# Kernel tuning notes

Hardware: AMD Instinct MI355X
Metric: run time of the kernel (lower is better)

The kernel has to match this reference:

```python
import jax, jax.numpy as jnp
import numpy as np

S, B, D, H = 2048, 2, 1024, 16
DK = D // H
SCALE = 1.0 / np.sqrt(DK)


def setup_inputs() -> dict:
    key = jax.random.key(0)
    ks = jax.random.split(key, 12)
    std = 1.0 / np.sqrt(D)
    inp = {
        "query": jax.random.normal(ks[0], (S, B, D), jnp.float32),
        "key": jax.random.normal(ks[1], (S, B, D), jnp.float32),
        "value": jax.random.normal(ks[2], (S, B, D), jnp.float32),
        # causal mask [S, S, 1]; mask[i, j] = 1 iff query i may attend key j
        "mask": jnp.tril(jnp.ones((S, S), jnp.bool_))[:, :, None],
        "Wq": jax.random.normal(ks[3], (D, D), jnp.float32) * std,
        "bq": jax.random.normal(ks[4], (D,), jnp.float32) * std,
        "Wk": jax.random.normal(ks[5], (D, D), jnp.float32) * std,
        "bk": jax.random.normal(ks[6], (D,), jnp.float32) * std,
        "Wv": jax.random.normal(ks[7], (D, D), jnp.float32) * std,
        "bv": jax.random.normal(ks[8], (D,), jnp.float32) * std,
        "Wo": jax.random.normal(ks[9], (D, D), jnp.float32) * std,
        "bo": jax.random.normal(ks[10], (D,), jnp.float32) * std,
    }
    return inp


def _proj(x, W, b):
    # nn.Linear: x @ W.T + b, then split into heads -> [S, B, H, DK]
    s, bsz, _ = x.shape
    y = jnp.einsum('sbd,ed->sbe', x, W) + b
    return y.reshape(s, bsz, H, DK)


def reference(query, key, value, mask, Wq, bq, Wk, bk, Wv, bv, Wo, bo):
    q = _proj(query, Wq, bq)   # [S,B,H,DK]
    k = _proj(key, Wk, bk)
    v = _proj(value, Wv, bv)
    scores = jnp.einsum('ibhd,jbhd->ijbh', q, k) * SCALE  # [S,S,B,H]
    m = mask[:, :, :, None]  # [S,S,1,1] or [S,S,B,1]
    scores = jnp.where(m, scores, jnp.float32(-1e9))
    attn = jax.nn.softmax(scores, axis=1)
    x = jnp.einsum('ijbh,jbhd->ibhd', attn, v)  # [S,B,H,DK]
    x = x.reshape(S, B, D)
    return jnp.einsum('sbd,ed->sbe', x, Wo) + bo
```

## Files before the change

### kernel.cpp

```cpp
#include <hip/hip_runtime.h>
#include <stdint.h>

#define S_LEN 2048
#define BATCH 2
#define DMODEL 1024
#define NHEAD 16
#define DHEAD 64
#define SCALE 0.125f

typedef float f32x4 __attribute__((ext_vector_type(4)));
typedef float f32x16 __attribute__((ext_vector_type(16)));
typedef __bf16 bf16x8 __attribute__((ext_vector_type(8)));

__device__ __forceinline__ unsigned short f2bf(float f) {
  union { float f; unsigned int u; } v;
  v.f = f;
  unsigned int u = v.u;
  return (unsigned short)((u + 0x7fffu + ((u >> 16) & 1u)) >> 16);
}

__device__ __forceinline__ void gld16(const void* g, void* l) {
  __builtin_amdgcn_global_load_lds((__attribute__((address_space(1))) void*)(g),
                                   (__attribute__((address_space(3))) void*)(l),
                                   16, 0, 0);
}

__global__ void cvt_all_kernel(const float* __restrict__ q, const float* __restrict__ k,
                               const float* __restrict__ v, const float* __restrict__ wq,
                               const float* __restrict__ wk, const float* __restrict__ wv,
                               const float* __restrict__ wosrc, unsigned short* __restrict__ xp,
                               unsigned short* __restrict__ wp, unsigned short* __restrict__ wo) {
  const int b = blockIdx.x;
  const float* src;
  unsigned short* dst;
  if (b < 12288) {
    const int z = b >> 12;
    const int local = b & 4095;
    src = (z == 0 ? q : (z == 1 ? k : v)) + (size_t)local * 1024;
    dst = xp + (size_t)z * 4194304 + (size_t)local * 1024;
  } else {
    const int z = (b - 12288) >> 10;
    const int local = (b - 12288) & 1023;
    src = (z == 0 ? wq : (z == 1 ? wk : (z == 2 ? wv : wosrc))) + (size_t)local * 1024;
    dst = (z < 3 ? wp + (size_t)z * 1048576 : wo) + (size_t)local * 1024;
  }
  const int i = threadIdx.x * 4;
  const float4 val = *(const float4*)(src + i);
  ushort4 o;
  o.x = f2bf(val.x); o.y = f2bf(val.y); o.z = f2bf(val.z); o.w = f2bf(val.w);
  *(ushort4*)(dst + i) = o;
}

template <int MODE>
__global__ __launch_bounds__(256, 2) void gemm_bt(
    const unsigned short* __restrict__ Abase,
    const unsigned short* __restrict__ Wbase,
    const float* __restrict__ bias0, const float* __restrict__ bias1,
    const float* __restrict__ bias2,
    unsigned short* __restrict__ qw, unsigned short* __restrict__ kw,
    unsigned short* __restrict__ vtw, float* __restrict__ outp) {
  constexpr int M = S_LEN * BATCH;
  constexpr int N = DMODEL;
  constexpr int K = DMODEL;
  __shared__ unsigned short At[128 * 32];
  __shared__ unsigned short Bt[128 * 32];

  const int m0 = blockIdx.x * 128;
  const int n0 = blockIdx.y * 128;
  const int z = (MODE == 0) ? blockIdx.z : 0;
  const unsigned short* A = Abase + (size_t)z * M * K;
  const unsigned short* W = Wbase + (size_t)z * N * K;
  const float* bias = (z == 0 ? bias0 : (z == 1 ? bias1 : bias2));

  const int tid = threadIdx.x;
  const int w = tid >> 6, l = tid & 63;
  const int wr = w >> 1, wc = w & 1;
  const int lr = l & 15, lg = l >> 4;

  const int srow = tid >> 2;
  const int scol = (tid & 3) * 8;

  f32x4 acc[4][4] = {};

  for (int k0 = 0; k0 < K; k0 += 32) {
    {
      const unsigned short* ga0 = A + (size_t)(m0 + srow) * K + k0 + scol;
      const unsigned short* ga1 = A + (size_t)(m0 + 64 + srow) * K + k0 + scol;
      const unsigned short* gb0 = W + (size_t)(n0 + srow) * K + k0 + scol;
      const unsigned short* gb1 = W + (size_t)(n0 + 64 + srow) * K + k0 + scol;
      char* la = (char*)At + w * 1024;
      char* lb = (char*)Bt + w * 1024;
      gld16(ga0, la);
      gld16(ga1, la + 4096);
      gld16(gb0, lb);
      gld16(gb1, lb + 4096);
    }
    __syncthreads();
    bf16x8 af[4], bfr[4];
#pragma unroll
    for (int mt = 0; mt < 4; ++mt)
      af[mt] = *(const bf16x8*)&At[(wr * 64 + mt * 16 + lr) * 32 + lg * 8];
#pragma unroll
    for (int nt = 0; nt < 4; ++nt)
      bfr[nt] = *(const bf16x8*)&Bt[(wc * 64 + nt * 16 + lr) * 32 + lg * 8];
#pragma unroll
    for (int mt = 0; mt < 4; ++mt)
#pragma unroll
      for (int nt = 0; nt < 4; ++nt)
        acc[mt][nt] = __builtin_amdgcn_mfma_f32_16x16x32_bf16(af[mt], bfr[nt], acc[mt][nt], 0, 0, 0);
    __syncthreads();
  }

#pragma unroll
  for (int mt = 0; mt < 4; ++mt) {
#pragma unroll
    for (int nt = 0; nt < 4; ++nt) {
#pragma unroll
      for (int r = 0; r < 4; ++r) {
        const int gm = m0 + wr * 64 + mt * 16 + lg * 4 + r;
        const int gn = n0 + wc * 64 + nt * 16 + lr;
        float v = acc[mt][nt][r] + bias[gn];
        if (MODE == 1) {
          outp[(size_t)gm * N + gn] = v;
        } else {
          if (z == 0) v *= SCALE;
          const int s = gm >> 1, bb = gm & 1;
          const int h = gn >> 6, dk = gn & 63;
          const int bh = bb * NHEAD + h;
          const unsigned short bv_ = f2bf(v);
          if (z == 0)
            qw[((size_t)bh * S_LEN + s) * DHEAD + dk] = bv_;
          else if (z == 1)
            kw[((size_t)bh * S_LEN + s) * DHEAD + dk] = bv_;
          else
            vtw[((size_t)bh * DHEAD + dk) * S_LEN + s] = bv_;
        }
      }
    }
  }
}

__global__ __launch_bounds__(128) void attn_kernel(
    const unsigned short* __restrict__ qw, const unsigned short* __restrict__ kw,
    const unsigned short* __restrict__ vtw, unsigned short* __restrict__ x2) {
  __shared__ unsigned short klds[64 * 64];
  __shared__ unsigned short vlds[64 * 64];

  const int qt = 31 - (int)blockIdx.x;
  const int bh = blockIdx.y;
  const int bb = bh >> 4, h = bh & 15;
  const int tid = threadIdx.x;
  const int w = tid >> 6, l = tid & 63;
  const int q5 = l & 31, hi = l >> 5;

  const size_t qkbase = (size_t)bh * S_LEN * DHEAD;
  const size_t vbase = (size_t)bh * DHEAD * S_LEN;

  const int qrow = qt * 64 + w * 32 + q5;
  bf16x8 qf[4];
#pragma unroll
  for (int d = 0; d < 4; ++d)
    qf[d] = *(const bf16x8*)&qw[qkbase + (size_t)qrow * DHEAD + d * 16 + hi * 8];

  f32x16 oacc0 = {}, oacc1 = {};
  float mrun = -1e30f, lrun = 0.f;

  for (int kt = 0; kt <= qt; ++kt) {
#pragma unroll
    for (int r = 0; r < 4; ++r) {
      const int id = r * 128 + tid;
      const int row = id >> 3;
      const int sw = (id & 7) ^ (row & 7);
      gld16(kw + qkbase + (size_t)(kt * 64 + row) * DHEAD + sw * 8,
            (char*)klds + r * 2048 + w * 1024);
      gld16(vtw + vbase + (size_t)row * S_LEN + kt * 64 + sw * 8,
            (char*)vlds + r * 2048 + w * 1024);
    }
    __syncthreads();

    f32x16 sA = {}, sB = {};
#pragma unroll
    for (int d = 0; d < 4; ++d) {
      const int ch = (2 * d + hi) ^ (q5 & 7);
      const bf16x8 kfA = *(const bf16x8*)((const char*)klds + q5 * 128 + ch * 16);
      const bf16x8 kfB = *(const bf16x8*)((const char*)klds + (32 + q5) * 128 + ch * 16);
      sA = __builtin_amdgcn_mfma_f32_32x32x16_bf16(kfA, qf[d], sA, 0, 0, 0);
      sB = __builtin_amdgcn_mfma_f32_32x32x16_bf16(kfB, qf[d], sB, 0, 0, 0);
    }

    if (kt == qt) {
      const int qloc = w * 32 + q5;
#pragma unroll
      for (int r = 0; r < 16; ++r) {
        const int kv = (r & 3) + 8 * (r >> 2) + 4 * hi;
        if (kv > qloc) sA[r] = -1e9f;
        if (kv + 32 > qloc) sB[r] = -1e9f;
      }
    }

    float tmax = sA[0];
#pragma unroll
    for (int r = 1; r < 16; ++r) tmax = fmaxf(tmax, sA[r]);
#pragma unroll
    for (int r = 0; r < 16; ++r) tmax = fmaxf(tmax, sB[r]);
    tmax = fmaxf(tmax, __shfl_xor(tmax, 32, 64));
    const float mnew = fmaxf(mrun, tmax);
    const float resc = __expf(mrun - mnew);
    mrun = mnew;
    float rsum = 0.f;
#pragma unroll
    for (int r = 0; r < 16; ++r) { sA[r] = __expf(sA[r] - mnew); rsum += sA[r]; }
#pragma unroll
    for (int r = 0; r < 16; ++r) { sB[r] = __expf(sB[r] - mnew); rsum += sB[r]; }
    rsum += __shfl_xor(rsum, 32, 64);
    lrun = lrun * resc + rsum;
#pragma unroll
    for (int r = 0; r < 16; ++r) { oacc0[r] *= resc; oacc1[r] *= resc; }

    unsigned pk[2][8];
#pragma unroll
    for (int g = 0; g < 4; ++g) {
      pk[0][2 * g]     = (unsigned)f2bf(sA[4 * g])     | ((unsigned)f2bf(sA[4 * g + 1]) << 16);
      pk[0][2 * g + 1] = (unsigned)f2bf(sA[4 * g + 2]) | ((unsigned)f2bf(sA[4 * g + 3]) << 16);
      pk[1][2 * g]     = (unsigned)f2bf(sB[4 * g])     | ((unsigned)f2bf(sB[4 * g + 1]) << 16);
      pk[1][2 * g + 1] = (unsigned)f2bf(sB[4 * g + 2]) | ((unsigned)f2bf(sB[4 * g + 3]) << 16);
    }

#pragma unroll
    for (int t = 0; t < 4; ++t) {
      const int c = t >> 1, ks = t & 1;
      const unsigned o0 = pk[c][4 * ks + 0], o1 = pk[c][4 * ks + 1];
      const unsigned o2 = pk[c][4 * ks + 2], o3 = pk[c][4 * ks + 3];
      const unsigned x0 = (unsigned)__shfl_xor((int)o0, 32, 64);
      const unsigned x1 = (unsigned)__shfl_xor((int)o1, 32, 64);
      const unsigned x2v = (unsigned)__shfl_xor((int)o2, 32, 64);
      const unsigned x3v = (unsigned)__shfl_xor((int)o3, 32, 64);
      union { unsigned u[4]; bf16x8 v; } pb;
      pb.u[0] = hi ? x2v : o0;
      pb.u[1] = hi ? x3v : o1;
      pb.u[2] = hi ? o2 : x0;
      pb.u[3] = hi ? o3 : x1;
      const int vch = (2 * t + hi) ^ (q5 & 7);
      const bf16x8 vf0 = *(const bf16x8*)((const char*)vlds + q5 * 128 + vch * 16);
      const bf16x8 vf1 = *(const bf16x8*)((const char*)vlds + (32 + q5) * 128 + vch * 16);
      oacc0 = __builtin_amdgcn_mfma_f32_32x32x16_bf16(vf0, pb.v, oacc0, 0, 0, 0);
      oacc1 = __builtin_amdgcn_mfma_f32_32x32x16_bf16(vf1, pb.v, oacc1, 0, 0, 0);
    }
    __syncthreads();
  }

  const float invl = 1.0f / lrun;
  const size_t obase = ((size_t)qrow * BATCH + bb) * DMODEL + h * DHEAD;
#pragma unroll
  for (int g = 0; g < 4; ++g) {
    const int d0 = 8 * g + 4 * hi;
    ushort4 s0, s1;
    s0.x = f2bf(oacc0[4 * g + 0] * invl);
    s0.y = f2bf(oacc0[4 * g + 1] * invl);
    s0.z = f2bf(oacc0[4 * g + 2] * invl);
    s0.w = f2bf(oacc0[4 * g + 3] * invl);
    s1.x = f2bf(oacc1[4 * g + 0] * invl);
    s1.y = f2bf(oacc1[4 * g + 1] * invl);
    s1.z = f2bf(oacc1[4 * g + 2] * invl);
    s1.w = f2bf(oacc1[4 * g + 3] * invl);
    *(ushort4*)(x2 + obase + d0) = s0;
    *(ushort4*)(x2 + obase + 32 + d0) = s1;
  }
}

extern "C" void kernel_launch(void* const* d_in, const int* in_sizes, int n_in,
                              void* d_out, int out_size, void* d_ws, size_t ws_size,
                              hipStream_t stream) {
  (void)in_sizes; (void)n_in; (void)out_size;
  if (ws_size < (size_t)67108864) return;

  const float* query = (const float*)d_in[0];
  const float* key_  = (const float*)d_in[1];
  const float* value = (const float*)d_in[2];
  const float* Wq = (const float*)d_in[4];
  const float* bq = (const float*)d_in[5];
  const float* Wk = (const float*)d_in[6];
  const float* bk = (const float*)d_in[7];
  const float* Wv = (const float*)d_in[8];
  const float* bv = (const float*)d_in[9];
  const float* Wo = (const float*)d_in[10];
  const float* bo = (const float*)d_in[11];

  char* ws = (char*)d_ws;
  unsigned short* xp = (unsigned short*)(ws);
  unsigned short* wp = (unsigned short*)(ws + 25165824);
  unsigned short* wo = (unsigned short*)(ws + 31457280);
  unsigned short* qws = (unsigned short*)(ws + 33554432);
  unsigned short* kws = (unsigned short*)(ws + 41943040);
  unsigned short* vtw = (unsigned short*)(ws + 50331648);
  unsigned short* x2 = (unsigned short*)(ws + 58720256);

  cvt_all_kernel<<<16384, 256, 0, stream>>>(query, key_, value, Wq, Wk, Wv, Wo, xp, wp, wo);

  gemm_bt<0><<<dim3(32, 8, 3), 256, 0, stream>>>(xp, wp, bq, bk, bv, qws, kws, vtw, nullptr);
  attn_kernel<<<dim3(32, 32), 128, 0, stream>>>(qws, kws, vtw, x2);
  gemm_bt<1><<<dim3(32, 8, 1), 256, 0, stream>>>(x2, wo, bo, bo, bo, nullptr, nullptr, nullptr,
                                                 (float*)d_out);
}
```

Measured before the change: 161.8 us.

## Pair causal query tiles per block, double-buffer K/V, use exp2 softmax

The attention kernel now handles two query tiles per block, a long one (31-x) and a short one (x), so every block does the same 33 KV iterations under the causal mask. K/V tiles are double-buffered in LDS so the next tile's global-to-LDS load overlaps the current tile's compute. The Q scale folds in log2(e) so softmax can use exp2f. It also adds tree reductions for max and sum, s_setprio around the MFMAs, and hardware bf16 packing. The cost is twice the LDS per block and half as many blocks (512), which may lower occupancy and latency hiding.

```diff
diff --git a/kernel.cpp b/kernel.cpp
--- a/kernel.cpp
+++ b/kernel.cpp
@@ -6,7 +6,7 @@
 #define DMODEL 1024
 #define NHEAD 16
 #define DHEAD 64
-#define SCALE 0.125f
+#define QSCALE 0.18033688011112042f
 
 typedef float f32x4 __attribute__((ext_vector_type(4)));
 typedef float f32x16 __attribute__((ext_vector_type(16)));
@@ -17,6 +17,12 @@
   v.f = f;
   unsigned int u = v.u;
   return (unsigned short)((u + 0x7fffu + ((u >> 16) & 1u)) >> 16);
+}
+
+__device__ __forceinline__ unsigned pk2(float lo, float hi_) {
+  union { __bf16 h[2]; unsigned u; } c;
+  c.h[0] = (__bf16)lo; c.h[1] = (__bf16)hi_;
+  return c.u;
 }
 
 __device__ __forceinline__ void gld16(const void* g, void* l) {
@@ -123,7 +129,7 @@
         if (MODE == 1) {
           outp[(size_t)gm * N + gn] = v;
         } else {
-          if (z == 0) v *= SCALE;
+          if (z == 0) v *= QSCALE;
           const int s = gm >> 1, bb = gm & 1;
           const int h = gn >> 6, dk = gn & 63;
           const int bh = bb * NHEAD + h;
@@ -143,11 +149,11 @@
 __global__ __launch_bounds__(128) void attn_kernel(
     const unsigned short* __restrict__ qw, const unsigned short* __restrict__ kw,
     const unsigned short* __restrict__ vtw, unsigned short* __restrict__ x2) {
-  __shared__ unsigned short klds[64 * 64];
-  __shared__ unsigned short vlds[64 * 64];
-
-  const int qt = 31 - (int)blockIdx.x;
-  const int bh = blockIdx.y;
+  __shared__ unsigned short klds[2][4096];
+  __shared__ unsigned short vlds[2][4096];
+
+  const int bh = blockIdx.x;
+  const int xpair = blockIdx.y;
   const int bb = bh >> 4, h = bh & 15;
   const int tid = threadIdx.x;
   const int w = tid >> 6, l = tid & 63;
@@ -156,37 +162,79 @@
   const size_t qkbase = (size_t)bh * S_LEN * DHEAD;
   const size_t vbase = (size_t)bh * DHEAD * S_LEN;
 
-  const int qrow = qt * 64 + w * 32 + q5;
-  bf16x8 qf[4];
-#pragma unroll
-  for (int d = 0; d < 4; ++d)
-    qf[d] = *(const bf16x8*)&qw[qkbase + (size_t)qrow * DHEAD + d * 16 + hi * 8];
-
-  f32x16 oacc0 = {}, oacc1 = {};
-  float mrun = -1e30f, lrun = 0.f;
-
-  for (int kt = 0; kt <= qt; ++kt) {
+  const int qtA = 31 - xpair, qtB = xpair;
+  const int nA = qtA + 1;
+  const int nit = nA + qtB + 1;
+
+  auto stage = [&](int kt, int b) {
 #pragma unroll
     for (int r = 0; r < 4; ++r) {
       const int id = r * 128 + tid;
       const int row = id >> 3;
       const int sw = (id & 7) ^ (row & 7);
       gld16(kw + qkbase + (size_t)(kt * 64 + row) * DHEAD + sw * 8,
-            (char*)klds + r * 2048 + w * 1024);
+            (char*)&klds[b][0] + r * 2048 + w * 1024);
       gld16(vtw + vbase + (size_t)row * S_LEN + kt * 64 + sw * 8,
-            (char*)vlds + r * 2048 + w * 1024);
-    }
-    __syncthreads();
-
-    f32x16 sA = {}, sB = {};
+            (char*)&vlds[b][0] + r * 2048 + w * 1024);
+    }
+  };
+
+  int qt = qtA;
+  int qrow = qt * 64 + w * 32 + q5;
+  bf16x8 qf[4];
+#pragma unroll
+  for (int d = 0; d < 4; ++d)
+    qf[d] = *(const bf16x8*)&qw[qkbase + (size_t)qrow * DHEAD + d * 16 + hi * 8];
+
+  f32x16 oacc0, oacc1;
+#pragma unroll
+  for (int r = 0; r < 16; ++r) { oacc0[r] = 0.f; oacc1[r] = 0.f; }
+  float mrun = -1e30f, lrun = 0.f;
+
+  auto flush = [&](int qr) {
+    const float invl = 1.0f / lrun;
+    const size_t obase = ((size_t)qr * BATCH + bb) * DMODEL + h * DHEAD;
+#pragma unroll
+    for (int g = 0; g < 4; ++g) {
+      const int d0 = 8 * g + 4 * hi;
+      ushort4 s0, s1;
+      s0.x = f2bf(oacc0[4 * g + 0] * invl);
+      s0.y = f2bf(oacc0[4 * g + 1] * invl);
+      s0.z = f2bf(oacc0[4 * g + 2] * invl);
+      s0.w = f2bf(oacc0[4 * g + 3] * invl);
+      s1.x = f2bf(oacc1[4 * g + 0] * invl);
+      s1.y = f2bf(oacc1[4 * g + 1] * invl);
+      s1.z = f2bf(oacc1[4 * g + 2] * invl);
+      s1.w = f2bf(oacc1[4 * g + 3] * invl);
+      *(ushort4*)(x2 + obase + d0) = s0;
+      *(ushort4*)(x2 + obase + 32 + d0) = s1;
+    }
+  };
+
+  stage(0, 0);
+  __syncthreads();
+
+  for (int i = 0; i < nit; ++i) {
+    const int cur = i & 1;
+    if (i + 1 < nit) {
+      const int nk = (i + 1 < nA) ? (i + 1) : (i + 1 - nA);
+      stage(nk, cur ^ 1);
+    }
+    const int kt = (i < nA) ? i : (i - nA);
+
+    f32x16 sA, sB;
+#pragma unroll
+    for (int r = 0; r < 16; ++r) { sA[r] = 0.f; sB[r] = 0.f; }
+    __builtin_amdgcn_s_setprio(1);
 #pragma unroll
     for (int d = 0; d < 4; ++d) {
       const int ch = (2 * d + hi) ^ (q5 & 7);
-      const bf16x8 kfA = *(const bf16x8*)((const char*)klds + q5 * 128 + ch * 16);
-      const bf16x8 kfB = *(const bf16x8*)((const char*)klds + (32 + q5) * 128 + ch * 16);
+      const bf16x8 kfA = *(const bf16x8*)((const char*)&klds[cur][0] + q5 * 128 + ch * 16);
+      const bf16x8 kfB = *(const bf16x8*)((const char*)&klds[cur][0] + (32 + q5) * 128 + ch * 16);
       sA = __builtin_amdgcn_mfma_f32_32x32x16_bf16(kfA, qf[d], sA, 0, 0, 0);
       sB = __builtin_amdgcn_mfma_f32_32x32x16_bf16(kfB, qf[d], sB, 0, 0, 0);
     }
+    __builtin_amdgcn_s_setprio(0);
 
     if (kt == qt) {
       const int qloc = w * 32 + q5;
@@ -198,20 +246,28 @@
       }
     }
 
-    float tmax = sA[0];
-#pragma unroll
-    for (int r = 1; r < 16; ++r) tmax = fmaxf(tmax, sA[r]);
-#pragma unroll
-    for (int r = 0; r < 16; ++r) tmax = fmaxf(tmax, sB[r]);
+    float mx[8];
+#pragma unroll
+    for (int j = 0; j < 8; ++j)
+      mx[j] = fmaxf(fmaxf(sA[j], sA[j + 8]), fmaxf(sB[j], sB[j + 8]));
+#pragma unroll
+    for (int j = 0; j < 4; ++j) mx[j] = fmaxf(mx[j], mx[j + 4]);
+    float tmax = fmaxf(fmaxf(mx[0], mx[1]), fmaxf(mx[2], mx[3]));
     tmax = fmaxf(tmax, __shfl_xor(tmax, 32, 64));
     const float mnew = fmaxf(mrun, tmax);
-    const float resc = __expf(mrun - mnew);
+    const float resc = exp2f(mrun - mnew);
     mrun = mnew;
-    float rsum = 0.f;
-#pragma unroll
-    for (int r = 0; r < 16; ++r) { sA[r] = __expf(sA[r] - mnew); rsum += sA[r]; }
-#pragma unroll
-    for (int r = 0; r < 16; ++r) { sB[r] = __expf(sB[r] - mnew); rsum += sB[r]; }
+#pragma unroll
+    for (int r = 0; r < 16; ++r) sA[r] = exp2f(sA[r] - mnew);
+#pragma unroll
+    for (int r = 0; r < 16; ++r) sB[r] = exp2f(sB[r] - mnew);
+    float sm[8];
+#pragma unroll
+    for (int j = 0; j < 8; ++j)
+      sm[j] = (sA[j] + sA[j + 8]) + (sB[j] + sB[j + 8]);
+#pragma unroll
+    for (int j = 0; j < 4; ++j) sm[j] += sm[j + 4];
+    float rsum = (sm[0] + sm[1]) + (sm[2] + sm[3]);
     rsum += __shfl_xor(rsum, 32, 64);
     lrun = lrun * resc + rsum;
 #pragma unroll
@@ -220,10 +276,10 @@
     unsigned pk[2][8];
 #pragma unroll
     for (int g = 0; g < 4; ++g) {
-      pk[0][2 * g]     = (unsigned)f2bf(sA[4 * g])     | ((unsigned)f2bf(sA[4 * g + 1]) << 16);
-      pk[0][2 * g + 1] = (unsigned)f2bf(sA[4 * g + 2]) | ((unsigned)f2bf(sA[4 * g + 3]) << 16);
-      pk[1][2 * g]     = (unsigned)f2bf(sB[4 * g])     | ((unsigned)f2bf(sB[4 * g + 1]) << 16);
-      pk[1][2 * g + 1] = (unsigned)f2bf(sB[4 * g + 2]) | ((unsigned)f2bf(sB[4 * g + 3]) << 16);
+      pk[0][2 * g]     = pk2(sA[4 * g],     sA[4 * g + 1]);
+      pk[0][2 * g + 1] = pk2(sA[4 * g + 2], sA[4 * g + 3]);
+      pk[1][2 * g]     = pk2(sB[4 * g],     sB[4 * g + 1]);
+      pk[1][2 * g + 1] = pk2(sB[4 * g + 2], sB[4 * g + 3]);
     }
 
 #pragma unroll
@@ -231,41 +287,40 @@
       const int c = t >> 1, ks = t & 1;
       const unsigned o0 = pk[c][4 * ks + 0], o1 = pk[c][4 * ks + 1];
       const unsigned o2 = pk[c][4 * ks + 2], o3 = pk[c][4 * ks + 3];
-      const unsigned x0 = (unsigned)__shfl_xor((int)o0, 32, 64);
-      const unsigned x1 = (unsigned)__shfl_xor((int)o1, 32, 64);
-      const unsigned x2v = (unsigned)__shfl_xor((int)o2, 32, 64);
-      const unsigned x3v = (unsigned)__shfl_xor((int)o3, 32, 64);
+      const unsigned e0 = (unsigned)__shfl_xor((int)o0, 32, 64);
+      const unsigned e1 = (unsigned)__shfl_xor((int)o1, 32, 64);
+      const unsigned e2 = (unsigned)__shfl_xor((int)o2, 32, 64);
+      const unsigned e3 = (unsigned)__shfl_xor((int)o3, 32, 64);
       union { unsigned u[4]; bf16x8 v; } pb;
-      pb.u[0] = hi ? x2v : o0;
-      pb.u[1] = hi ? x3v : o1;
-      pb.u[2] = hi ? o2 : x0;
-      pb.u[3] = hi ? o3 : x1;
+      pb.u[0] = hi ? e2 : o0;
+      pb.u[1] = hi ? e3 : o1;
+      pb.u[2] = hi ? o2 : e0;
+      pb.u[3] = hi ? o3 : e1;
       const int vch = (2 * t + hi) ^ (q5 & 7);
-      const bf16x8 vf0 = *(const bf16x8*)((const char*)vlds + q5 * 128 + vch * 16);
-      const bf16x8 vf1 = *(const bf16x8*)((const char*)vlds + (32 + q5) * 128 + vch * 16);
+      const bf16x8 vf0 = *(const bf16x8*)((const char*)&vlds[cur][0] + q5 * 128 + vch * 16);
+      const bf16x8 vf1 = *(const bf16x8*)((const char*)&vlds[cur][0] + (32 + q5) * 128 + vch * 16);
+      __builtin_amdgcn_s_setprio(1);
       oacc0 = __builtin_amdgcn_mfma_f32_32x32x16_bf16(vf0, pb.v, oacc0, 0, 0, 0);
       oacc1 = __builtin_amdgcn_mfma_f32_32x32x16_bf16(vf1, pb.v, oacc1, 0, 0, 0);
+      __builtin_amdgcn_s_setprio(0);
+    }
+
+    if (i == nA - 1) {
+      flush(qrow);
+      qt = qtB;
+      qrow = qt * 64 + w * 32 + q5;
+#pragma unroll
+      for (int d = 0; d < 4; ++d)
+        qf[d] = *(const bf16x8*)&qw[qkbase + (size_t)qrow * DHEAD + d * 16 + hi * 8];
+#pragma unroll
+      for (int r = 0; r < 16; ++r) { oacc0[r] = 0.f; oacc1[r] = 0.f; }
+      mrun = -1e30f;
+      lrun = 0.f;
     }
     __syncthreads();
   }
 
-  const float invl = 1.0f / lrun;
-  const size_t obase = ((size_t)qrow * BATCH + bb) * DMODEL + h * DHEAD;
-#pragma unroll
-  for (int g = 0; g < 4; ++g) {
-    const int d0 = 8 * g + 4 * hi;
-    ushort4 s0, s1;
-    s0.x = f2bf(oacc0[4 * g + 0] * invl);
-    s0.y = f2bf(oacc0[4 * g + 1] * invl);
-    s0.z = f2bf(oacc0[4 * g + 2] * invl);
-    s0.w = f2bf(oacc0[4 * g + 3] * invl);
-    s1.x = f2bf(oacc1[4 * g + 0] * invl);
-    s1.y = f2bf(oacc1[4 * g + 1] * invl);
-    s1.z = f2bf(oacc1[4 * g + 2] * invl);
-    s1.w = f2bf(oacc1[4 * g + 3] * invl);
-    *(ushort4*)(x2 + obase + d0) = s0;
-    *(ushort4*)(x2 + obase + 32 + d0) = s1;
-  }
+  flush(qrow);
 }
 
 extern "C" void kernel_launch(void* const* d_in, const int* in_sizes, int n_in,
@@ -298,7 +353,7 @@
   cvt_all_kernel<<<16384, 256, 0, stream>>>(query, key_, value, Wq, Wk, Wv, Wo, xp, wp, wo);
 
   gemm_bt<0><<<dim3(32, 8, 3), 256, 0, stream>>>(xp, wp, bq, bk, bv, qws, kws, vtw, nullptr);
-  attn_kernel<<<dim3(32, 32), 128, 0, stream>>>(qws, kws, vtw, x2);
+  attn_kernel<<<dim3(32, 16), 128, 0, stream>>>(qws, kws, vtw, x2);
   gemm_bt<1><<<dim3(32, 8, 1), 256, 0, stream>>>(x2, wo, bo, bo, bo, nullptr, nullptr, nullptr,
                                                  (float*)d_out);
 }
```

New measurement: 166.7 us. +3.0%, slower.
